# Performance work log

Measured on AMD Instinct MI355X. Metric: run time of the kernel, lower is better.

## Reference

```python
import jax, jax.numpy as jnp
import numpy as np

B, S, D, H, HD, C = 4, 1024, 1024, 16, 64, 64
NC = S // C
DFF = 4 * HD
BASE_LR = 1.0
EPS = 1e-6

def _ln(x, g, b, eps=EPS):
    mu = jnp.mean(x, axis=-1, keepdims=True)
    var = jnp.mean((x - mu) ** 2, axis=-1, keepdims=True)
    return (x - mu) * jax.lax.rsqrt(var + eps) * g + b

def _gelu(x):
    return 0.5 * x * (1.0 + jnp.tanh(0.79788456 * (x + 0.044715 * x * x * x)))

def _gelu_bwd(x):
    t = jnp.tanh(0.79788456 * (x + 0.044715 * x * x * x))
    return 0.5 * x * (1.0 - t * t) * (0.79788456 + 0.1070322243 * x * x) + 0.5 * (1.0 + t)

def _ln_l2_bwd(x, tgt, g, b, eps=EPS):
    # grad of 0.5*||LN_affine(x) - tgt||^2 w.r.t. x (fused layernorm backward)
    d = x.shape[-1]
    mu = jnp.mean(x, axis=-1, keepdims=True)
    var = jnp.mean((x - mu) ** 2, axis=-1, keepdims=True)
    std = jnp.sqrt(var + eps)
    xh = (x - mu) / std
    gh = (g * xh + b - tgt) * g
    return (d * gh - jnp.sum(gh, axis=-1, keepdims=True) - xh * jnp.sum(gh * xh, axis=-1, keepdims=True)) / (d * std)

def setup_inputs():
    key = jax.random.key(0)
    ks = jax.random.split(key, 16)
    n = lambda k, shape, s=0.02: jax.random.normal(k, shape, dtype=jnp.float32) * s
    return {
        "x": jax.random.normal(ks[0], (B, S, D), dtype=jnp.float32),
        "ln1_w": jnp.ones((D,), jnp.float32), "ln1_b": jnp.zeros((D,), jnp.float32),
        "attn_wq": n(ks[1], (D, D)), "attn_wk": n(ks[2], (D, D)),
        "attn_wv": n(ks[3], (D, D)), "attn_wo": n(ks[4], (D, D)),
        "wq_w": n(ks[5], (D, D)), "wq_b": jnp.zeros((D,), jnp.float32),
        "wk_w": n(ks[6], (D, D)), "wk_b": jnp.zeros((D,), jnp.float32),
        "wv_w": n(ks[7], (D, D)), "wv_b": jnp.zeros((D,), jnp.float32),
        "wo_w": n(ks[8], (D, D)), "wo_b": jnp.zeros((D,), jnp.float32),
        "W1": n(ks[9], (H, HD, DFF)), "b1": jnp.zeros((H, 1, DFF), jnp.float32),
        "W2": n(ks[10], (H, DFF, HD)), "b2": jnp.zeros((H, 1, HD), jnp.float32),
        "ttt_nw": jnp.ones((H, HD), jnp.float32), "ttt_nb": jnp.zeros((H, HD), jnp.float32),
        "lr_w": n(ks[11], (H, 1, D)), "lr_b": jnp.zeros((H, 1), jnp.float32),
        "pn_w": jnp.ones((D,), jnp.float32), "pn_b": jnp.zeros((D,), jnp.float32),
        "gate_alpha": n(ks[12], (D,)),
    }

def reference(x, ln1_w, ln1_b, attn_wq, attn_wk, attn_wv, attn_wo,
              wq_w, wq_b, wk_w, wk_b, wv_w, wv_b, wo_w, wo_b,
              W1, b1, W2, b2, ttt_nw, ttt_nb, lr_w, lr_b, pn_w, pn_b, gate_alpha):
    # ---- self-attention block (pre-norm, causal, residual) ----
    h = _ln(x, ln1_w, ln1_b)
    q = (h @ attn_wq.T).reshape(B, S, H, HD)
    k = (h @ attn_wk.T).reshape(B, S, H, HD)
    v = (h @ attn_wv.T).reshape(B, S, H, HD)
    scores = jnp.einsum('bqhd,bkhd->bhqk', q, k) / jnp.float32(np.sqrt(HD))
    causal = jnp.tril(jnp.ones((S, S), bool))
    scores = jnp.where(causal, scores, jnp.float32(-1e30))
    o = jnp.einsum('bhqk,bkhd->bqhd', jax.nn.softmax(scores, axis=-1), v).reshape(B, S, D)
    x = x + o @ attn_wo.T

    # ---- TTT-MLP chunked inner-loop (Video-DiT style) ----
    residual = x
    XQ = (x @ wq_w.T + wq_b).reshape(B, S, H, HD)
    XK = (x @ wk_w.T + wk_b).reshape(B, S, H, HD)
    XV = (x @ wv_w.T + wv_b).reshape(B, S, H, HD)
    XQ = XQ / jnp.maximum(jnp.linalg.norm(XQ, axis=-1, keepdims=True), 1e-12)
    XK = XK / jnp.maximum(jnp.linalg.norm(XK, axis=-1, keepdims=True), 1e-12)
    # ln reconstruction target: affine-LN(XV) + XK
    XV = ttt_nw[None, None] * _ln(XV, 1.0, 0.0) + ttt_nb[None, None] + XK

    to_ttt = lambda t: jnp.moveaxis(t.reshape(B, NC, C, H, HD), 3, 1)  # [B,H,NC,C,HD]
    XQc, XKc, XVc = to_ttt(XQ), to_ttt(XK), to_ttt(XV)

    xc = x.reshape(B, NC, C, D)
    ttt_lr = jax.nn.sigmoid(jnp.einsum('bnkc,hdc->bhnkd', xc, lr_w) + lr_b.reshape(1, H, 1, 1, 1))
    eta = BASE_LR * jnp.swapaxes(ttt_lr, -1, -2) / HD  # [B,H,NC,1,C]

    gW = ttt_nw[None, :, None, :]
    gB = ttt_nb[None, :, None, :]

    def step(carry, inp):
        W1s, b1s, W2s, b2s = carry
        xq, xk, xv, et = inp                          # [B,H,C,HD], et [B,H,1,C]
        eta_mb = jnp.broadcast_to(et, (B, H, C, C))
        Z1 = xk @ W1s + b1s                           # [B,H,C,DFF]
        X2 = _gelu(Z1)
        Z2 = X2 @ W2s + b2s                           # [B,H,C,HD]
        gZ2 = _ln_l2_bwd(Z2, xv - xk, gW, gB)
        gZ1 = (gZ2 @ jnp.swapaxes(W2s, -1, -2)) * _gelu_bwd(Z1)
        eta_tril = jnp.tril(eta_mb)
        A1 = jnp.tril(xq @ jnp.swapaxes(xk, -1, -2))
        Z1b = xq @ W1s - (eta_mb * A1) @ gZ1 + (b1s - eta_tril @ gZ1)
        X2b = _gelu(Z1b)
        A2 = jnp.tril(X2b @ jnp.swapaxes(X2, -1, -2))
        Z2b = X2b @ W2s - (eta_mb * A2) @ gZ2 + (b2s - eta_tril @ gZ2)
        last = eta_mb[:, :, -1, :, None]              # [B,H,C,1]
        W1n = W1s - jnp.swapaxes(last * xk, -1, -2) @ gZ1
        b1n = b1s - jnp.sum(last * gZ1, axis=-2, keepdims=True)
        W2n = W2s - jnp.swapaxes(last * X2, -1, -2) @ gZ2
        b2n = b2s - jnp.sum(last * gZ2, axis=-2, keepdims=True)
        out = xq + _ln(Z2b, gW, gB)
        return (W1n, b1n, W2n, b2n), out

    carry = (jnp.broadcast_to(W1, (B, H, HD, DFF)), jnp.broadcast_to(b1, (B, H, 1, DFF)),
             jnp.broadcast_to(W2, (B, H, DFF, HD)), jnp.broadcast_to(b2, (B, H, 1, HD)))
    xs = tuple(jnp.moveaxis(t, 2, 0) for t in (XQc, XKc, XVc, eta))
    _, outs = jax.lax.scan(step, carry, xs)           # [NC,B,H,C,HD]
    ttt_out = outs.transpose(1, 0, 3, 2, 4).reshape(B, S, D)

    z = _ln(ttt_out, pn_w, pn_b) @ wo_w.T + wo_b      # post-norm then output proj
    return residual + jnp.tanh(gate_alpha) * z        # SSM gating + gated residual
```

## Files before the change

kernel.cpp:

```cpp
#include <hip/hip_runtime.h>

typedef short v8s __attribute__((ext_vector_type(8)));
typedef short v4s __attribute__((ext_vector_type(4)));
typedef float v4f __attribute__((ext_vector_type(4)));

__device__ __forceinline__ float bfu(unsigned short u){ return __uint_as_float(((unsigned)u)<<16); }
__device__ __forceinline__ unsigned short fbf(float f){
  unsigned u = __float_as_uint(f);
  u += 0x7fffu + ((u>>16)&1u);
  return (unsigned short)(u>>16);
}
__device__ __forceinline__ float wsum(float v){
  #pragma unroll
  for (int off=32; off>0; off>>=1) v += __shfl_xor(v, off, 64);
  return v;
}
__device__ __forceinline__ float clampv(float x){ return fminf(fmaxf(x, -1e8f), 1e8f); }
__device__ __forceinline__ float tanh_f(float x){
  x = fminf(fmaxf(x, -15.f), 15.f);
  float e = __expf(2.f*x);
  return (e-1.f)/(e+1.f);
}
__device__ __forceinline__ float gelu_f(float x){
  float t = tanh_f(0.79788456f*(x + 0.044715f*x*x*x));
  return 0.5f*x*(1.f+t);
}
__device__ __forceinline__ float gelu_bwd_f(float x){
  float t = tanh_f(0.79788456f*(x + 0.044715f*x*x*x));
  return 0.5f*x*(1.f-t*t)*(0.79788456f + 0.1070322243f*x*x) + 0.5f*(1.f+t);
}
__device__ __forceinline__ v8s ld8(const unsigned short* p){
  v4s lo = *(const v4s*)p, hi = *(const v4s*)(p+4);
  v8s r;
  r[0]=lo[0];r[1]=lo[1];r[2]=lo[2];r[3]=lo[3];
  r[4]=hi[0];r[5]=hi[1];r[6]=hi[2];r[7]=hi[3];
  return r;
}

__global__ __launch_bounds__(256) void wcvt_kernel(
    const float* __restrict__ s0, const float* __restrict__ s1, const float* __restrict__ s2,
    unsigned short* __restrict__ d0, unsigned short* __restrict__ d1, unsigned short* __restrict__ d2)
{
  int y = blockIdx.y;
  const float* s = y==0?s0:(y==1?s1:s2);
  unsigned short* d = y==0?d0:(y==1?d1:d2);
  int tid = blockIdx.x*256 + threadIdx.x;
  #pragma unroll 4
  for (int i=0;i<16;i++){
    size_t o = (size_t)i*65536 + (size_t)tid*4;
    float4 v = *(const float4*)&s[o];
    v4s p;
    p[0]=(short)fbf(v.x); p[1]=(short)fbf(v.y); p[2]=(short)fbf(v.z); p[3]=(short)fbf(v.w);
    *(v4s*)&d[o] = p;
  }
}

__global__ __launch_bounds__(256) void ln_kernel(
    const float* __restrict__ X, const float* __restrict__ g,
    const float* __restrict__ bta, float* __restrict__ out,
    unsigned short* __restrict__ outbf)
{
  __shared__ float red[4];
  int row = blockIdx.x, t = threadIdx.x;
  const float* xr = X + (size_t)row*1024;
  float v[4];
  #pragma unroll
  for (int i=0;i<4;i++) v[i] = xr[t + i*256];
  float s = v[0]+v[1]+v[2]+v[3];
  s = wsum(s);
  if ((t&63)==0) red[t>>6]=s;
  __syncthreads();
  float mu = (red[0]+red[1]+red[2]+red[3])*(1.f/1024.f);
  float q=0.f;
  #pragma unroll
  for (int i=0;i<4;i++){ float dd=v[i]-mu; q+=dd*dd; }
  q = wsum(q);
  __syncthreads();
  if ((t&63)==0) red[t>>6]=q;
  __syncthreads();
  float var = (red[0]+red[1]+red[2]+red[3])*(1.f/1024.f);
  float rs = rsqrtf(var+1e-6f);
  #pragma unroll
  for (int i=0;i<4;i++){
    int c = t+i*256;
    float vv = (v[i]-mu)*rs*g[c] + bta[c];
    if (out)   out[(size_t)row*1024+c] = vv;
    if (outbf) outbf[(size_t)row*1024+c] = fbf(vv);
  }
}

__global__ __launch_bounds__(256, 2) void gemm_kernel(
    const unsigned short* __restrict__ A_bf,
    const unsigned short* __restrict__ B0, const unsigned short* __restrict__ B1, const unsigned short* __restrict__ B2,
    const float* __restrict__ bias0, const float* __restrict__ bias1, const float* __restrict__ bias2,
    const float* __restrict__ res, const float* __restrict__ gate,
    float* __restrict__ out0, float* __restrict__ out1, float* __restrict__ out2,
    unsigned short* __restrict__ obf0, unsigned short* __restrict__ obf1, unsigned short* __restrict__ obf2)
{
  __shared__ __attribute__((aligned(16))) unsigned short a_lds[128*68];
  __shared__ __attribute__((aligned(16))) unsigned short b_lds[128*68];
  int t=threadIdx.x, w=t>>6, lane=t&63;
  int widx = blockIdx.x>>3;
  const unsigned short* Bw = widx==0?B0:(widx==1?B1:B2);
  const float* bias = widx==0?bias0:(widx==1?bias1:bias2);
  float* out        = widx==0?out0:(widx==1?out1:out2);
  unsigned short* obf = widx==0?obf0:(widx==1?obf1:obf2);
  int gm = blockIdx.y*128, gn = (blockIdx.x&7)*128;
  int wm=(w>>1)*64, wn=(w&1)*64, lr=lane&15, lk=(lane>>4)*8;
  v4f acc[4][4];
  #pragma unroll
  for (int i=0;i<4;i++)
    #pragma unroll
    for (int j=0;j<4;j++){ v4f z={0.f,0.f,0.f,0.f}; acc[i][j]=z; }
  for (int kk=0; kk<1024; kk+=64){
    __syncthreads();
    #pragma unroll
    for (int i=0;i<4;i++){
      int slot=i*256+t, row=slot>>3, c8=(slot&7)*8;
      const unsigned short* srcA=&A_bf[(size_t)(gm+row)*1024 + kk + c8];
      v4s lo=*(const v4s*)srcA, hi=*(const v4s*)(srcA+4);
      *(v4s*)&a_lds[row*68+c8]   = lo;
      *(v4s*)&a_lds[row*68+c8+4] = hi;
      const unsigned short* srcB=&Bw[(size_t)(gn+row)*1024 + kk + c8];
      v4s blo=*(const v4s*)srcB, bhi=*(const v4s*)(srcB+4);
      *(v4s*)&b_lds[row*68+c8]   = blo;
      *(v4s*)&b_lds[row*68+c8+4] = bhi;
    }
    __syncthreads();
    #pragma unroll
    for (int k2=0;k2<2;k2++){
      v8s af[4], bfr[4];
      #pragma unroll
      for (int i=0;i<4;i++) af[i] = ld8(&a_lds[(wm+i*16+lr)*68 + k2*32+lk]);
      #pragma unroll
      for (int j=0;j<4;j++) bfr[j] = ld8(&b_lds[(wn+j*16+lr)*68 + k2*32+lk]);
      #pragma unroll
      for (int i=0;i<4;i++)
        #pragma unroll
        for (int j=0;j<4;j++)
          acc[i][j] = __builtin_amdgcn_mfma_f32_16x16x32_bf16(af[i], bfr[j], acc[i][j], 0,0,0);
    }
  }
  int quad = lane>>4;
  #pragma unroll
  for (int j=0;j<4;j++){
    int gc = gn + wn + j*16 + lr;
    float bval = bias ? bias[gc] : 0.f;
    float gval = gate ? tanh_f(gate[gc]) : 1.f;
    #pragma unroll
    for (int i=0;i<4;i++){
      #pragma unroll
      for (int r=0;r<4;r++){
        int grow = gm + wm + i*16 + quad*4 + r;
        float v = (acc[i][j][r] + bval)*gval;
        if (res) v += res[(size_t)grow*1024 + gc];
        size_t oi = (size_t)grow*1024 + gc;
        if (out) out[oi] = v;
        if (obf) obf[oi] = fbf(v);
      }
    }
  }
}

__global__ __launch_bounds__(256) void attn_kernel(
    const unsigned short* __restrict__ Q, const unsigned short* __restrict__ K,
    const unsigned short* __restrict__ V, float* __restrict__ O,
    unsigned short* __restrict__ Obf)
{
  __shared__ __attribute__((aligned(16))) unsigned short q_l[64*68];
  __shared__ __attribute__((aligned(16))) unsigned short k_l[64*68];
  __shared__ __attribute__((aligned(16))) unsigned short vt_l[64*68];
  __shared__ __attribute__((aligned(16))) unsigned short p_l[64*68];
  int t=threadIdx.x, w=t>>6, lane=t&63, q=lane>>4, l16=lane&15;
  int qt = blockIdx.x & 15, bh = blockIdx.x >> 4;
  int b = bh >> 4, h = bh & 15;
  const size_t base = ((size_t)b*1024)*1024 + (size_t)h*64;
  #pragma unroll
  for (int pass=0;pass<4;pass++){
    int slot=t+pass*256, row=slot>>4, c4=(slot&15)*4;
    v4s qv = *(const v4s*)&Q[base + (size_t)(qt*64+row)*1024 + c4];
    *(v4s*)&q_l[row*68+c4]=qv;
  }
  float mi[4], li[4];
  v4f o[4];
  #pragma unroll
  for (int r=0;r<4;r++){ mi[r]=-1e30f; li[r]=0.f; }
  #pragma unroll
  for (int dtn=0;dtn<4;dtn++){ v4f z={0.f,0.f,0.f,0.f}; o[dtn]=z; }
  for (int kt=0; kt<=qt; kt++){
    __syncthreads();
    #pragma unroll
    for (int pass=0;pass<4;pass++){
      int slot=t+pass*256, row=slot>>4, c4=(slot&15)*4;
      v4s kv = *(const v4s*)&K[base + (size_t)(kt*64+row)*1024 + c4];
      *(v4s*)&k_l[row*68+c4]=kv;
      v4s vv = *(const v4s*)&V[base + (size_t)(kt*64+row)*1024 + c4];
      vt_l[(c4+0)*68+row]=(unsigned short)vv[0];
      vt_l[(c4+1)*68+row]=(unsigned short)vv[1];
      vt_l[(c4+2)*68+row]=(unsigned short)vv[2];
      vt_l[(c4+3)*68+row]=(unsigned short)vv[3];
    }
    __syncthreads();
    v4f s[4];
    #pragma unroll
    for (int nt=0;nt<4;nt++){ v4f z={0.f,0.f,0.f,0.f}; s[nt]=z; }
    #pragma unroll
    for (int k2=0;k2<2;k2++){
      v8s af = ld8(&q_l[(w*16+l16)*68 + k2*32+q*8]);
      #pragma unroll
      for (int nt=0;nt<4;nt++){
        v8s bf = ld8(&k_l[(nt*16+l16)*68 + k2*32+q*8]);
        s[nt] = __builtin_amdgcn_mfma_f32_16x16x32_bf16(af, bf, s[nt], 0,0,0);
      }
    }
    bool diag = (kt==qt);
    #pragma unroll
    for (int r=0;r<4;r++){
      int row_l = w*16+q*4+r;
      float mx=-1e30f;
      #pragma unroll
      for (int nt=0;nt<4;nt++){
        int col=nt*16+l16;
        float sv = s[nt][r]*0.125f;
        if (diag && col>row_l) sv=-1e30f;
        s[nt][r]=sv; mx=fmaxf(mx,sv);
      }
      #pragma unroll
      for (int off=1;off<16;off<<=1) mx=fmaxf(mx,__shfl_xor(mx,off,16));
      float mnew=fmaxf(mi[r],mx);
      float aexp=__expf(mi[r]-mnew);
      float ps=0.f;
      #pragma unroll
      for (int nt=0;nt<4;nt++){
        float p=__expf(s[nt][r]-mnew);
        s[nt][r]=p; ps+=p;
      }
      #pragma unroll
      for (int off=1;off<16;off<<=1) ps+=__shfl_xor(ps,off,16);
      li[r]=li[r]*aexp+ps; mi[r]=mnew;
      #pragma unroll
      for (int dtn=0;dtn<4;dtn++) o[dtn][r]*=aexp;
      #pragma unroll
      for (int nt=0;nt<4;nt++) p_l[row_l*68 + nt*16+l16]=fbf(s[nt][r]);
    }
    __syncthreads();
    #pragma unroll
    for (int k2=0;k2<2;k2++){
      v8s af = ld8(&p_l[(w*16+l16)*68 + k2*32+q*8]);
      #pragma unroll
      for (int dtn=0;dtn<4;dtn++){
        v8s bf = ld8(&vt_l[(dtn*16+l16)*68 + k2*32+q*8]);
        o[dtn] = __builtin_amdgcn_mfma_f32_16x16x32_bf16(af, bf, o[dtn], 0,0,0);
      }
    }
  }
  #pragma unroll
  for (int dtn=0;dtn<4;dtn++)
    #pragma unroll
    for (int r=0;r<4;r++){
      float vv = o[dtn][r]/li[r];
      size_t oi = base + (size_t)(qt*64+w*16+q*4+r)*1024 + dtn*16+l16;
      if (O)   O[oi] = vv;
      if (Obf) Obf[oi] = fbf(vv);
    }
}

__global__ __launch_bounds__(256) void xqkv_kernel(
    const float* __restrict__ XQ, const float* __restrict__ XK,
    const float* __restrict__ XV, const float* __restrict__ nw,
    const float* __restrict__ nb, const float* __restrict__ eta,
    float* __restrict__ xqt, float* __restrict__ tgtp,
    unsigned short* __restrict__ xq_bf, unsigned short* __restrict__ xk_bf,
    unsigned short* __restrict__ xkTe_bf)
{
  int gw = (int)((blockIdx.x*256 + threadIdx.x)>>6);
  int lane = threadIdx.x & 63;
  int h = gw & 15, s = (gw>>4)&1023, b = gw>>14;
  size_t src = ((size_t)(b*1024+s))*1024 + h*64 + lane;
  float xq = XQ[src], xk = XK[src], xv = XV[src];
  float nq = sqrtf(wsum(xq*xq));
  float nk = sqrtf(wsum(xk*xk));
  float xqn = xq / fmaxf(nq, 1e-12f);
  float xkn = xk / fmaxf(nk, 1e-12f);
  float mu = wsum(xv)*(1.f/64.f);
  float xm = xv-mu;
  float var = wsum(xm*xm)*(1.f/64.f);
  float xvh = xm*rsqrtf(var+1e-6f);
  float tg = nw[h*64+lane]*xvh + nb[h*64+lane];
  float et = eta[((size_t)(b*16+h))*1024 + s];
  size_t dst = ((size_t)(b*16+h)*1024 + s)*64 + lane;
  xq_bf[dst]=fbf(xqn); xk_bf[dst]=fbf(xkn);
  xkTe_bf[((size_t)(b*16+h)*64 + lane)*1024 + s] = fbf(-et*xkn);
  int n_ = s>>6, row = s&63;
  int wv = row>>4, qq = (row>>2)&3, rr = row&3;
  int nt_ = lane>>4, l16_ = lane&15;
  int tt = wv*64 + qq*16 + l16_;
  size_t dst2 = (size_t)(b*16+h)*65536 + (size_t)n_*4096 + (size_t)tt*16 + nt_*4 + rr;
  xqt[dst2]=xqn; tgtp[dst2]=tg;
}

__global__ __launch_bounds__(256) void eta_kernel(
    const float* __restrict__ Xb, const float* __restrict__ lrw,
    const float* __restrict__ lrb, float* __restrict__ eta)
{
  int gw = (int)((blockIdx.x*256 + threadIdx.x)>>6);
  int lane = threadIdx.x & 63;
  int s = gw & 1023, b = gw >> 10;
  const float* xrow = Xb + ((size_t)(b*1024+s))*1024;
  float xr[16];
  #pragma unroll
  for (int i=0;i<16;i++) xr[i] = xrow[i*64+lane];
  #pragma unroll 1
  for (int h=0;h<16;h++){
    const float* wr = lrw + h*1024;
    float acc=0.f;
    #pragma unroll
    for (int i=0;i<16;i++) acc += xr[i]*wr[i*64+lane];
    acc = wsum(acc);
    if (lane==h){
      float vv = acc + lrb[h];
      float sg = 1.f/(1.f+__expf(-vv));
      eta[((size_t)(b*16+h))*1024 + s] = sg*(1.f/64.f);
    }
  }
}

__global__ __launch_bounds__(512, 2) __attribute__((amdgpu_waves_per_eu(2, 2)))
void scan_kernel(
    const float* __restrict__ xqt, const float* __restrict__ tgtp,
    const unsigned short* __restrict__ xq_bf, const unsigned short* __restrict__ xk_bf,
    const unsigned short* __restrict__ xkTe_bf, const float* __restrict__ eta,
    const float* __restrict__ W1in, const float* __restrict__ b1in,
    const float* __restrict__ W2in, const float* __restrict__ b2in,
    const float* __restrict__ nw, const float* __restrict__ nb,
    float* __restrict__ tout)
{
  __shared__ __attribute__((aligned(16))) unsigned short W1t[256*68];
  __shared__ __attribute__((aligned(16))) unsigned short W2T[64*260];
  __shared__ __attribute__((aligned(16))) unsigned short X2s[64*260];
  __shared__ __attribute__((aligned(16))) unsigned short GXu[256*68];
  __shared__ __attribute__((aligned(16))) unsigned short GZ2t[64*68];
  __shared__ __attribute__((aligned(16))) unsigned short AMs[64*68];
  __shared__ float ln_scr[64*8];
  __shared__ float eta_s[64], b1_s[256], b2_s[64], nw_s[64], nb_s[64];

  const int t=threadIdx.x, w=t>>6, lane=t&63, q=lane>>4, l16=lane&15;
  const int bh=blockIdx.x, b=bh>>4, h=bh&15;
  const int mt=w>>1, half=w&1, nh=half*8, nh4=half*2;
  const float* xq_g  = xqt  + (size_t)bh*65536;
  const float* tgt_g = tgtp + (size_t)bh*65536;
  const unsigned short* xqb_g = xq_bf  + (size_t)bh*65536;
  const unsigned short* xkb_g = xk_bf  + (size_t)bh*65536;
  const unsigned short* xkT_g = xkTe_bf + (size_t)bh*65536;
  const float* eta_g = eta + (size_t)bh*1024;

  v4f w1r[8];
  #pragma unroll
  for (int nt=0;nt<8;nt++){
    int col=(nh+nt)*16+l16;
    #pragma unroll
    for (int r=0;r<4;r++) w1r[nt][r] = W1in[h*16384 + (mt*16+q*4+r)*256 + col];
  }
  v4f w2r[2][4];
  #pragma unroll
  for (int mi=0;mi<2;mi++)
    #pragma unroll
    for (int nt=0;nt<4;nt++){
      int col=nt*16+l16;
      #pragma unroll
      for (int r=0;r<4;r++) w2r[mi][nt][r] = W2in[h*16384 + ((w*2+mi)*16+q*4+r)*64 + col];
    }
  if (t<256) b1_s[t]=b1in[h*256+t];
  if (t<64){ b2_s[t]=b2in[h*64+t]; nw_s[t]=nw[h*64+t]; nb_s[t]=nb[h*64+t]; }

  float bacc=0.f, bacc2=0.f;

  for (int n=0;n<16;n++){
    v8s xkf[2], xqf[2];
    #pragma unroll
    for (int kt=0;kt<2;kt++){
      xkf[kt] = ld8(&xkb_g[(size_t)n*4096 + (mt*16+l16)*64 + kt*32+q*8]);
      xqf[kt] = ld8(&xqb_g[(size_t)n*4096 + (mt*16+l16)*64 + kt*32+q*8]);
    }
    __syncthreads();
    if (t<256) b1_s[t] -= bacc;
    if (t<64){ b2_s[t] -= bacc2; eta_s[t]=eta_g[n*64+t]; }
    #pragma unroll
    for (int nt=0;nt<8;nt++){
      int col=(nh+nt)*16+l16;
      #pragma unroll
      for (int pr=0;pr<2;pr++){
        unsigned lo=fbf(w1r[nt][pr*2]), hi=fbf(w1r[nt][pr*2+1]);
        *(unsigned*)&W1t[col*68 + mt*16+q*4 + pr*2] = lo | (hi<<16);
      }
    }
    #pragma unroll
    for (int mi=0;mi<2;mi++)
      #pragma unroll
      for (int nt=0;nt<4;nt++){
        int col=nt*16+l16;
        #pragma unroll
        for (int pr=0;pr<2;pr++){
          unsigned lo=fbf(w2r[mi][nt][pr*2]), hi=fbf(w2r[mi][nt][pr*2+1]);
          *(unsigned*)&W2T[col*260 + (w*2+mi)*16+q*4 + pr*2] = lo | (hi<<16);
        }
      }
    __syncthreads();

    unsigned gbp[16];
    {
      v4f a1[8];
      #pragma unroll
      for (int i=0;i<8;i++){ v4f z={0.f,0.f,0.f,0.f}; a1[i]=z; }
      #pragma unroll
      for (int kt=0;kt<2;kt++){
        #pragma unroll
        for (int nt=0;nt<8;nt++){
          v8s bf = ld8(&W1t[((nh+nt)*16+l16)*68 + kt*32+q*8]);
          a1[nt] = __builtin_amdgcn_mfma_f32_16x16x32_bf16(xkf[kt], bf, a1[nt], 0,0,0);
        }
      }
      #pragma unroll
      for (int nt=0;nt<8;nt++){
        int col=(nh+nt)*16+l16; float bb=b1_s[col];
        float zz[4];
        #pragma unroll
        for (int r=0;r<4;r++){
          float z=clampv(a1[nt][r]+bb); zz[r]=z;
          X2s[(mt*16+q*4+r)*260+col]=fbf(clampv(gelu_f(z)));
        }
        #pragma unroll
        for (int pr=0;pr<2;pr++)
          gbp[nt*2+pr] = (unsigned)fbf(gelu_bwd_f(zz[pr*2+0]))
                       | ((unsigned)fbf(gelu_bwd_f(zz[pr*2+1]))<<16);
      }
    }
    {
      v4f a4[2];
      #pragma unroll
      for (int i=0;i<2;i++){ v4f z={0.f,0.f,0.f,0.f}; a4[i]=z; }
      #pragma unroll
      for (int kt=0;kt<2;kt++){
        #pragma unroll
        for (int nt=0;nt<2;nt++){
          v8s bf = ld8(&xkb_g[(size_t)n*4096 + ((nh4+nt)*16+l16)*64 + kt*32+q*8]);
          a4[nt] = __builtin_amdgcn_mfma_f32_16x16x32_bf16(xqf[kt], bf, a4[nt], 0,0,0);
        }
      }
      #pragma unroll
      for (int nt=0;nt<2;nt++){
        int col=(nh4+nt)*16+l16;
        float ec=eta_s[col];
        #pragma unroll
        for (int r=0;r<4;r++){
          int row=mt*16+q*4+r;
          AMs[row*68+col] = (col<=row) ? fbf(-ec*(a4[nt][r]+1.f)) : (unsigned short)0;
        }
      }
    }

    {
      const float* tc = tgt_g + (size_t)n*4096 + (size_t)(mt*64+q*16+l16)*16 + nh4*4;
      float4 ta=*(const float4*)tc, tb=*(const float4*)(tc+4);
      float tgs[8]={ta.x,ta.y,ta.z,ta.w,tb.x,tb.y,tb.z,tb.w};
      v4f a2[2];
      #pragma unroll
      for (int i=0;i<2;i++){ v4f z={0.f,0.f,0.f,0.f}; a2[i]=z; }
      #pragma unroll
      for (int kt=0;kt<8;kt++){
        v8s af = ld8(&X2s[(mt*16+l16)*260 + kt*32+q*8]);
        #pragma unroll
        for (int nt=0;nt<2;nt++){
          v8s bf = ld8(&W2T[((nh4+nt)*16+l16)*260 + kt*32+q*8]);
          a2[nt] = __builtin_amdgcn_mfma_f32_16x16x32_bf16(af, bf, a2[nt], 0,0,0);
        }
      }
      float z2[2][4];
      #pragma unroll
      for (int nt=0;nt<2;nt++){
        float bb=b2_s[(nh4+nt)*16+l16];
        #pragma unroll
        for (int r=0;r<4;r++) z2[nt][r]=clampv(a2[nt][r]+bb);
      }
      #pragma unroll
      for (int r=0;r<4;r++){
        float s1v=z2[0][r]+z2[1][r];
        float s2v=z2[0][r]*z2[0][r]+z2[1][r]*z2[1][r];
        #pragma unroll
        for (int off=1;off<16;off<<=1){ s1v+=__shfl_xor(s1v,off,16); s2v+=__shfl_xor(s2v,off,16); }
        if (l16==0){ int row=mt*16+q*4+r; ln_scr[row*8+half]=s1v; ln_scr[row*8+2+half]=s2v; }
      }
      __syncthreads();
      float muv[4], istd[4];
      #pragma unroll
      for (int r=0;r<4;r++){
        int row=mt*16+q*4+r;
        float S1=ln_scr[row*8+0]+ln_scr[row*8+1];
        float S2=ln_scr[row*8+2]+ln_scr[row*8+3];
        float mu=S1*(1.f/64.f);
        float var=fmaxf(S2*(1.f/64.f)-mu*mu, 0.f);
        muv[r]=mu; istd[r]=rsqrtf(var+1e-6f);
      }
      float xh[2][4], gh[2][4];
      #pragma unroll
      for (int nt=0;nt<2;nt++){
        int col=(nh4+nt)*16+l16;
        float gw_=nw_s[col], gb_=nb_s[col];
        #pragma unroll
        for (int r=0;r<4;r++){
          float x_=(z2[nt][r]-muv[r])*istd[r];
          float tgv = tgs[nt*4+r];
          xh[nt][r]=x_;
          gh[nt][r]=(gw_*x_+gb_-tgv)*gw_;
        }
      }
      #pragma unroll
      for (int r=0;r<4;r++){
        float t1=gh[0][r]+gh[1][r];
        float t2=gh[0][r]*xh[0][r]+gh[1][r]*xh[1][r];
        #pragma unroll
        for (int off=1;off<16;off<<=1){ t1+=__shfl_xor(t1,off,16); t2+=__shfl_xor(t2,off,16); }
        if (l16==0){ int row=mt*16+q*4+r; ln_scr[row*8+4+half]=t1; ln_scr[row*8+6+half]=t2; }
      }
      __syncthreads();
      #pragma unroll
      for (int nt=0;nt<2;nt++){
        int col=(nh4+nt)*16+l16;
        #pragma unroll
        for (int pr=0;pr<2;pr++){
          unsigned pk[2];
          #pragma unroll
          for (int k2=0;k2<2;k2++){
            int r=pr*2+k2;
            int row=mt*16+q*4+r;
            float G1s=ln_scr[row*8+4]+ln_scr[row*8+5];
            float G2s=ln_scr[row*8+6]+ln_scr[row*8+7];
            float gz=(64.f*gh[nt][r]-G1s-xh[nt][r]*G2s)*istd[r]*(1.f/64.f);
            pk[k2]=fbf(clampv(gz));
          }
          *(unsigned*)&GZ2t[col*68 + mt*16+q*4 + pr*2] = pk[0] | (pk[1]<<16);
        }
      }
    }
    __syncthreads();

    {
      v4f a3[8];
      #pragma unroll
      for (int i=0;i<8;i++){ v4f z={0.f,0.f,0.f,0.f}; a3[i]=z; }
      #pragma unroll
      for (int kt=0;kt<2;kt++){
        v8s af;
        #pragma unroll
        for (int j=0;j<8;j++) af[j]=(short)GZ2t[(kt*32+q*8+j)*68 + mt*16+l16];
        #pragma unroll
        for (int nt=0;nt<8;nt++){
          int nb0=(nh+nt)*16+l16;
          v8s bf;
          #pragma unroll
          for (int j=0;j<8;j++) bf[j]=(short)W2T[(kt*32+q*8+j)*260 + nb0];
          a3[nt] = __builtin_amdgcn_mfma_f32_16x16x32_bf16(af, bf, a3[nt], 0,0,0);
        }
      }
      #pragma unroll
      for (int nt=0;nt<8;nt++){
        int col=(nh+nt)*16+l16;
        #pragma unroll
        for (int pr=0;pr<2;pr++){
          float d0=bfu((unsigned short)(gbp[nt*2+pr]&0xffffu));
          float d1=bfu((unsigned short)(gbp[nt*2+pr]>>16));
          float g0=clampv(a3[nt][pr*2+0]*d0);
          float g1=clampv(a3[nt][pr*2+1]*d1);
          unsigned lo=fbf(g0), hi=fbf(g1);
          *(unsigned*)&GXu[col*68 + mt*16+q*4 + pr*2] = lo | (hi<<16);
        }
      }
    }
    __syncthreads();

    unsigned x2bp[16];
    {
      float p0=0.f,p1=0.f,p2=0.f,p3=0.f;
      if (t<256){
        #pragma unroll
        for (int j4=0;j4<16;j4++){
          v4s v=*(const v4s*)&GXu[t*68+j4*4];
          p0 += eta_s[j4*4+0]*bfu((unsigned short)v[0]);
          p1 += eta_s[j4*4+1]*bfu((unsigned short)v[1]);
          p2 += eta_s[j4*4+2]*bfu((unsigned short)v[2]);
          p3 += eta_s[j4*4+3]*bfu((unsigned short)v[3]);
        }
      }
      bacc=(p0+p1)+(p2+p3);
      v8s xef[2];
      #pragma unroll
      for (int kt=0;kt<2;kt++)
        xef[kt] = ld8(&xkT_g[(size_t)(mt*16+l16)*1024 + n*64 + kt*32+q*8]);
      v4f a5[8];
      #pragma unroll
      for (int i=0;i<8;i++){ v4f z={0.f,0.f,0.f,0.f}; a5[i]=z; }
      #pragma unroll
      for (int kt=0;kt<2;kt++){
        #pragma unroll
        for (int nt=0;nt<8;nt++){
          v8s bf = ld8(&W1t[((nh+nt)*16+l16)*68 + kt*32+q*8]);
          a5[nt] = __builtin_amdgcn_mfma_f32_16x16x32_bf16(xqf[kt], bf, a5[nt], 0,0,0);
        }
      }
      #pragma unroll
      for (int kt=0;kt<2;kt++){
        v8s afA = ld8(&AMs[(mt*16+l16)*68 + kt*32+q*8]);
        #pragma unroll
        for (int nt=0;nt<8;nt++){
          v8s bf = ld8(&GXu[((nh+nt)*16+l16)*68 + kt*32+q*8]);
          a5[nt] = __builtin_amdgcn_mfma_f32_16x16x32_bf16(afA, bf, a5[nt], 0,0,0);
          w1r[nt] = __builtin_amdgcn_mfma_f32_16x16x32_bf16(xef[kt], bf, w1r[nt], 0,0,0);
        }
      }
      #pragma unroll
      for (int nt=0;nt<8;nt++){
        float bb=b1_s[(nh+nt)*16+l16];
        #pragma unroll
        for (int pr=0;pr<2;pr++){
          float z0=clampv(a5[nt][pr*2+0]+bb);
          float z1=clampv(a5[nt][pr*2+1]+bb);
          x2bp[nt*2+pr] = (unsigned)fbf(clampv(gelu_f(z0)))
                        | ((unsigned)fbf(clampv(gelu_f(z1)))<<16);
        }
      }
    }
    __syncthreads();

    #pragma unroll
    for (int nt=0;nt<8;nt++){
      int col=(nh+nt)*16+l16;
      #pragma unroll
      for (int pr=0;pr<2;pr++){
        int row0=mt*16+q*4+pr*2;
        GXu[row0*260+col]     = (unsigned short)(x2bp[nt*2+pr]&0xffffu);
        GXu[(row0+1)*260+col] = (unsigned short)(x2bp[nt*2+pr]>>16);
      }
    }
    __syncthreads();

    {
      float p0=0.f,p1=0.f,p2=0.f,p3=0.f;
      if (t<64){
        #pragma unroll
        for (int j4=0;j4<16;j4++){
          v4s v=*(const v4s*)&GZ2t[t*68+j4*4];
          p0 += eta_s[j4*4+0]*bfu((unsigned short)v[0]);
          p1 += eta_s[j4*4+1]*bfu((unsigned short)v[1]);
          p2 += eta_s[j4*4+2]*bfu((unsigned short)v[2]);
          p3 += eta_s[j4*4+3]*bfu((unsigned short)v[3]);
        }
      }
      bacc2=(p0+p1)+(p2+p3);
      v4f a7[2];
      #pragma unroll
      for (int i=0;i<2;i++){ v4f z={0.f,0.f,0.f,0.f}; a7[i]=z; }
      #pragma unroll
      for (int kt=0;kt<8;kt++){
        v8s af = ld8(&GXu[(mt*16+l16)*260 + kt*32+q*8]);
        #pragma unroll
        for (int nt=0;nt<2;nt++){
          v8s bf = ld8(&X2s[((nh4+nt)*16+l16)*260 + kt*32+q*8]);
          a7[nt] = __builtin_amdgcn_mfma_f32_16x16x32_bf16(af, bf, a7[nt], 0,0,0);
        }
      }
      #pragma unroll
      for (int nt=0;nt<2;nt++){
        int col=(nh4+nt)*16+l16;
        float ec=eta_s[col];
        #pragma unroll
        for (int r=0;r<4;r++){
          int row=mt*16+q*4+r;
          AMs[row*68+col] = (col<=row) ? fbf(-ec*(a7[nt][r]+1.f)) : (unsigned short)0;
        }
      }
    }
    __syncthreads();

    {
      const float* xc = xq_g + (size_t)n*4096 + (size_t)(mt*64+q*16+l16)*16 + nh4*4;
      float4 xa=*(const float4*)xc, xb=*(const float4*)(xc+4);
      float xqs[8]={xa.x,xa.y,xa.z,xa.w,xb.x,xb.y,xb.z,xb.w};
      v4f a8[2];
      #pragma unroll
      for (int i=0;i<2;i++){ v4f z={0.f,0.f,0.f,0.f}; a8[i]=z; }
      float b2old[2];
      #pragma unroll
      for (int nt=0;nt<2;nt++) b2old[nt]=b2_s[(nh4+nt)*16+l16];
      #pragma unroll
      for (int kt=0;kt<8;kt++){
        v8s af = ld8(&GXu[(mt*16+l16)*260 + kt*32+q*8]);
        #pragma unroll
        for (int nt=0;nt<2;nt++){
          v8s bf = ld8(&W2T[((nh4+nt)*16+l16)*260 + kt*32+q*8]);
          a8[nt] = __builtin_amdgcn_mfma_f32_16x16x32_bf16(af, bf, a8[nt], 0,0,0);
        }
      }
      #pragma unroll
      for (int kt=0;kt<2;kt++){
        v8s afm = ld8(&AMs[(mt*16+l16)*68 + kt*32+q*8]);
        #pragma unroll
        for (int nt=0;nt<2;nt++){
          v8s bf = ld8(&GZ2t[((nh4+nt)*16+l16)*68 + kt*32+q*8]);
          a8[nt] = __builtin_amdgcn_mfma_f32_16x16x32_bf16(afm, bf, a8[nt], 0,0,0);
        }
      }
      float z2b[2][4];
      #pragma unroll
      for (int nt=0;nt<2;nt++)
        #pragma unroll
        for (int r=0;r<4;r++) z2b[nt][r]=clampv(a8[nt][r]+b2old[nt]);
      #pragma unroll
      for (int r=0;r<4;r++){
        float s1v=z2b[0][r]+z2b[1][r];
        float s2v=z2b[0][r]*z2b[0][r]+z2b[1][r]*z2b[1][r];
        #pragma unroll
        for (int off=1;off<16;off<<=1){ s1v+=__shfl_xor(s1v,off,16); s2v+=__shfl_xor(s2v,off,16); }
        if (l16==0){ int row=mt*16+q*4+r; ln_scr[row*8+half]=s1v; ln_scr[row*8+2+half]=s2v; }
      }
      __syncthreads();
      #pragma unroll
      for (int r=0;r<4;r++){
        int row=mt*16+q*4+r;
        float S1=ln_scr[row*8+0]+ln_scr[row*8+1];
        float S2=ln_scr[row*8+2]+ln_scr[row*8+3];
        float mu=S1*(1.f/64.f);
        float var=fmaxf(S2*(1.f/64.f)-mu*mu, 0.f);
        float istd=rsqrtf(var+1e-6f);
        #pragma unroll
        for (int nt=0;nt<2;nt++){
          int col=(nh4+nt)*16+l16;
          float x_=(z2b[nt][r]-mu)*istd;
          float outv = xqs[nt*4+r] + x_*nw_s[col] + nb_s[col];
          tout[((size_t)(b*1024 + n*64 + row))*1024 + h*64 + col] = outv;
        }
      }
      #pragma unroll
      for (int kt=0;kt<2;kt++){
        v8s bfs[4];
        #pragma unroll
        for (int nt=0;nt<4;nt++) bfs[nt] = ld8(&GZ2t[(nt*16+l16)*68 + kt*32+q*8]);
        #pragma unroll
        for (int mi=0;mi<2;mi++){
          v8s af;
          #pragma unroll
          for (int j=0;j<8;j++){
            int jj=kt*32+q*8+j;
            af[j]=(short)fbf(-eta_s[jj]*bfu(X2s[jj*260 + (w*2+mi)*16+l16]));
          }
          #pragma unroll
          for (int nt=0;nt<4;nt++)
            w2r[mi][nt] = __builtin_amdgcn_mfma_f32_16x16x32_bf16(af, bfs[nt], w2r[mi][nt], 0,0,0);
        }
      }
    }
  }
}

extern "C" void kernel_launch(void* const* d_in, const int* in_sizes, int n_in,
                              void* d_out, int out_size, void* d_ws, size_t ws_size,
                              hipStream_t stream)
{
  const float* x_in   = (const float*)d_in[0];
  const float* ln1w   = (const float*)d_in[1];
  const float* ln1b   = (const float*)d_in[2];
  const float* awq    = (const float*)d_in[3];
  const float* awk    = (const float*)d_in[4];
  const float* awv    = (const float*)d_in[5];
  const float* awo    = (const float*)d_in[6];
  const float* wqw    = (const float*)d_in[7];
  const float* wqb    = (const float*)d_in[8];
  const float* wkw    = (const float*)d_in[9];
  const float* wkb    = (const float*)d_in[10];
  const float* wvw    = (const float*)d_in[11];
  const float* wvb    = (const float*)d_in[12];
  const float* wow    = (const float*)d_in[13];
  const float* wob    = (const float*)d_in[14];
  const float* W1in   = (const float*)d_in[15];
  const float* b1in   = (const float*)d_in[16];
  const float* W2in   = (const float*)d_in[17];
  const float* b2in   = (const float*)d_in[18];
  const float* tnw    = (const float*)d_in[19];
  const float* tnb    = (const float*)d_in[20];
  const float* lrw    = (const float*)d_in[21];
  const float* lrb    = (const float*)d_in[22];
  const float* pnw    = (const float*)d_in[23];
  const float* pnb    = (const float*)d_in[24];
  const float* galpha = (const float*)d_in[25];
  float* outp = (float*)d_out;
  char* ws = (char*)d_ws;
  const size_t MB = (size_t)1<<20;
  float* bq  = (float*)(ws + 0*MB);
  float* bk  = (float*)(ws + 16*MB);
  float* bv  = (float*)(ws + 32*MB);
  float* bo  = (float*)(ws + 64*MB);
  float* bxb = (float*)(ws + 80*MB);
  float* xqt = (float*)(ws + 96*MB);
  float* tgtp = (float*)(ws + 112*MB);
  unsigned short* xq_bf  = (unsigned short*)(ws + 128*MB);
  unsigned short* xk_bf  = (unsigned short*)(ws + 136*MB);
  float* etab = (float*)(ws + 144*MB);
  unsigned short* xkTe_bf = (unsigned short*)(ws + 48*MB);
  unsigned short* wc0 = (unsigned short*)(ws + 56*MB);
  unsigned short* wc1 = (unsigned short*)(ws + 58*MB);
  unsigned short* wc2 = (unsigned short*)(ws + 60*MB);
  unsigned short* bhh_bf  = (unsigned short*)(ws + 96*MB);
  unsigned short* bq_bf   = (unsigned short*)(ws + 128*MB);
  unsigned short* bk_bf   = (unsigned short*)(ws + 136*MB);
  unsigned short* bv_bf   = (unsigned short*)(ws + 80*MB);
  unsigned short* bo_bf   = (unsigned short*)(ws + 112*MB);
  unsigned short* bxb_bf  = (unsigned short*)(ws + 128*MB);
  unsigned short* bhh2_bf = (unsigned short*)(ws + 0*MB);
  float* tout = bo;

  wcvt_kernel<<<dim3(64,3),256,0,stream>>>(awq,awk,awv, wc0,wc1,wc2);
  ln_kernel<<<4096,256,0,stream>>>(x_in, ln1w, ln1b, nullptr, bhh_bf);
  gemm_kernel<<<dim3(24,32),256,0,stream>>>(bhh_bf, wc0,wc1,wc2,
      nullptr,nullptr,nullptr, nullptr, nullptr,
      nullptr,nullptr,nullptr, bq_bf,bk_bf,bv_bf);
  wcvt_kernel<<<dim3(64,1),256,0,stream>>>(awo,nullptr,nullptr, wc0,nullptr,nullptr);
  attn_kernel<<<1024,256,0,stream>>>(bq_bf,bk_bf,bv_bf, nullptr, bo_bf);
  gemm_kernel<<<dim3(8,32),256,0,stream>>>(bo_bf, wc0,wc0,wc0,
      nullptr,nullptr,nullptr, x_in, nullptr,
      bxb,bxb,bxb, bxb_bf,bxb_bf,bxb_bf);
  wcvt_kernel<<<dim3(64,3),256,0,stream>>>(wqw,wkw,wvw, wc0,wc1,wc2);
  gemm_kernel<<<dim3(24,32),256,0,stream>>>(bxb_bf, wc0,wc1,wc2,
      wqb,wkb,wvb, nullptr, nullptr,
      bq,bk,bv, nullptr,nullptr,nullptr);
  wcvt_kernel<<<dim3(64,1),256,0,stream>>>(wow,nullptr,nullptr, wc0,nullptr,nullptr);
  eta_kernel<<<1024,256,0,stream>>>(bxb, lrw, lrb, etab);
  xqkv_kernel<<<16384,256,0,stream>>>(bq,bk,bv,tnw,tnb,etab,xqt,tgtp,xq_bf,xk_bf,xkTe_bf);
  scan_kernel<<<64,512,0,stream>>>(xqt,tgtp,xq_bf,xk_bf,xkTe_bf,etab,W1in,b1in,W2in,b2in,tnw,tnb,tout);
  ln_kernel<<<4096,256,0,stream>>>(tout, pnw, pnb, nullptr, bhh2_bf);
  gemm_kernel<<<dim3(8,32),256,0,stream>>>(bhh2_bf, wc0,wc0,wc0,
      wob,wob,wob, bxb, galpha,
      outp,outp,outp, nullptr,nullptr,nullptr);
}
```

Measured before the change: 926.7 us.

## Fuse scan layernorm-backward reductions into one pass and merge weight conversions

The layernorm-backward in the sequential scan kernel is rewritten algebraically so the row sums needed for the gradient (sum of gh and gh*xhat) come from raw moments gathered in the same shuffle reduction as mean and variance. This removes a second shuffle reduction and one block barrier per chunk. The change also hoists the target, xq and transposed-xk loads to the top of each chunk iteration, computes tanh once for both GELU and its derivative, and merges the separate output-weight conversion launches into the four-way convert kernels. The trade-off is slightly different floating-point rounding from the expanded moment formulas, plus higher register pressure from the hoisted loads.

```diff
diff --git a/kernel.cpp b/kernel.cpp
--- a/kernel.cpp
+++ b/kernel.cpp
@@ -38,12 +38,14 @@
 }
 
 __global__ __launch_bounds__(256) void wcvt_kernel(
-    const float* __restrict__ s0, const float* __restrict__ s1, const float* __restrict__ s2,
-    unsigned short* __restrict__ d0, unsigned short* __restrict__ d1, unsigned short* __restrict__ d2)
+    const float* __restrict__ s0, const float* __restrict__ s1,
+    const float* __restrict__ s2, const float* __restrict__ s3,
+    unsigned short* __restrict__ d0, unsigned short* __restrict__ d1,
+    unsigned short* __restrict__ d2, unsigned short* __restrict__ d3)
 {
   int y = blockIdx.y;
-  const float* s = y==0?s0:(y==1?s1:s2);
-  unsigned short* d = y==0?d0:(y==1?d1:d2);
+  const float* s = y==0?s0:(y==1?s1:(y==2?s2:s3));
+  unsigned short* d = y==0?d0:(y==1?d1:(y==2?d2:d3));
   int tid = blockIdx.x*256 + threadIdx.x;
   #pragma unroll 4
   for (int i=0;i<16;i++){
@@ -341,7 +343,7 @@
   __shared__ __attribute__((aligned(16))) unsigned short GXu[256*68];
   __shared__ __attribute__((aligned(16))) unsigned short GZ2t[64*68];
   __shared__ __attribute__((aligned(16))) unsigned short AMs[64*68];
-  __shared__ float ln_scr[64*8];
+  __shared__ float ln_scr[64*12];
   __shared__ float eta_s[64], b1_s[256], b2_s[64], nw_s[64], nb_s[64];
 
   const int t=threadIdx.x, w=t>>6, lane=t&63, q=lane>>4, l16=lane&15;
@@ -372,15 +374,31 @@
     }
   if (t<256) b1_s[t]=b1in[h*256+t];
   if (t<64){ b2_s[t]=b2in[h*64+t]; nw_s[t]=nw[h*64+t]; nb_s[t]=nb[h*64+t]; }
+  __syncthreads();
+  float T2g=0.f;
+  #pragma unroll
+  for (int c=0;c<64;c++){ float g=nw_s[c]; T2g += g*g; }
 
   float bacc=0.f, bacc2=0.f;
 
   for (int n=0;n<16;n++){
-    v8s xkf[2], xqf[2];
+    v8s xkf[2], xqf[2], xef[2];
     #pragma unroll
     for (int kt=0;kt<2;kt++){
       xkf[kt] = ld8(&xkb_g[(size_t)n*4096 + (mt*16+l16)*64 + kt*32+q*8]);
       xqf[kt] = ld8(&xqb_g[(size_t)n*4096 + (mt*16+l16)*64 + kt*32+q*8]);
+      xef[kt] = ld8(&xkT_g[(size_t)(mt*16+l16)*1024 + n*64 + kt*32+q*8]);
+    }
+    float tgs[8], xqs[8];
+    {
+      const float* tc = tgt_g + (size_t)n*4096 + (size_t)(mt*64+q*16+l16)*16 + nh4*4;
+      float4 ta=*(const float4*)tc, tb=*(const float4*)(tc+4);
+      tgs[0]=ta.x;tgs[1]=ta.y;tgs[2]=ta.z;tgs[3]=ta.w;
+      tgs[4]=tb.x;tgs[5]=tb.y;tgs[6]=tb.z;tgs[7]=tb.w;
+      const float* xc = xq_g + (size_t)n*4096 + (size_t)(mt*64+q*16+l16)*16 + nh4*4;
+      float4 xa=*(const float4*)xc, xb=*(const float4*)(xc+4);
+      xqs[0]=xa.x;xqs[1]=xa.y;xqs[2]=xa.z;xqs[3]=xa.w;
+      xqs[4]=xb.x;xqs[5]=xb.y;xqs[6]=xb.z;xqs[7]=xb.w;
     }
     __syncthreads();
     if (t<256) b1_s[t] -= bacc;
@@ -423,16 +441,18 @@
       #pragma unroll
       for (int nt=0;nt<8;nt++){
         int col=(nh+nt)*16+l16; float bb=b1_s[col];
-        float zz[4];
+        unsigned short dbf[4];
         #pragma unroll
         for (int r=0;r<4;r++){
-          float z=clampv(a1[nt][r]+bb); zz[r]=z;
-          X2s[(mt*16+q*4+r)*260+col]=fbf(clampv(gelu_f(z)));
-        }
-        #pragma unroll
-        for (int pr=0;pr<2;pr++)
-          gbp[nt*2+pr] = (unsigned)fbf(gelu_bwd_f(zz[pr*2+0]))
-                       | ((unsigned)fbf(gelu_bwd_f(zz[pr*2+1]))<<16);
+          float z=clampv(a1[nt][r]+bb);
+          float tt = tanh_f(0.79788456f*(z + 0.044715f*z*z*z));
+          float ge = 0.5f*z*(1.f+tt);
+          float gd = 0.5f*z*(1.f-tt*tt)*(0.79788456f + 0.1070322243f*z*z) + 0.5f*(1.f+tt);
+          X2s[(mt*16+q*4+r)*260+col]=fbf(clampv(ge));
+          dbf[r]=fbf(gd);
+        }
+        gbp[nt*2+0] = (unsigned)dbf[0] | ((unsigned)dbf[1]<<16);
+        gbp[nt*2+1] = (unsigned)dbf[2] | ((unsigned)dbf[3]<<16);
       }
     }
     {
@@ -460,9 +480,6 @@
     }
 
     {
-      const float* tc = tgt_g + (size_t)n*4096 + (size_t)(mt*64+q*16+l16)*16 + nh4*4;
-      float4 ta=*(const float4*)tc, tb=*(const float4*)(tc+4);
-      float tgs[8]={ta.x,ta.y,ta.z,ta.w,tb.x,tb.y,tb.z,tb.w};
       v4f a2[2];
       #pragma unroll
       for (int i=0;i<2;i++){ v4f z={0.f,0.f,0.f,0.f}; a2[i]=z; }
@@ -476,70 +493,57 @@
         }
       }
       float z2[2][4];
-      #pragma unroll
-      for (int nt=0;nt<2;nt++){
-        float bb=b2_s[(nh4+nt)*16+l16];
-        #pragma unroll
-        for (int r=0;r<4;r++) z2[nt][r]=clampv(a2[nt][r]+bb);
+      float gw0=nw_s[(nh4+0)*16+l16], gw1=nw_s[(nh4+1)*16+l16];
+      float gb0=nb_s[(nh4+0)*16+l16], gb1=nb_s[(nh4+1)*16+l16];
+      float gw20=gw0*gw0, gw21=gw1*gw1;
+      {
+        float bb0=b2_s[(nh4+0)*16+l16], bb1=b2_s[(nh4+1)*16+l16];
+        #pragma unroll
+        for (int r=0;r<4;r++){ z2[0][r]=clampv(a2[0][r]+bb0); z2[1][r]=clampv(a2[1][r]+bb1); }
       }
       #pragma unroll
       for (int r=0;r<4;r++){
-        float s1v=z2[0][r]+z2[1][r];
-        float s2v=z2[0][r]*z2[0][r]+z2[1][r]*z2[1][r];
-        #pragma unroll
-        for (int off=1;off<16;off<<=1){ s1v+=__shfl_xor(s1v,off,16); s2v+=__shfl_xor(s2v,off,16); }
-        if (l16==0){ int row=mt*16+q*4+r; ln_scr[row*8+half]=s1v; ln_scr[row*8+2+half]=s2v; }
+        float z0=z2[0][r], z1=z2[1][r];
+        float a0=gw0*(gb0-tgs[r]), a1v=gw1*(gb1-tgs[4+r]);
+        float s1=z0+z1, s2=z0*z0+z1*z1;
+        float t1=gw20*z0+gw21*z1;
+        float t4=gw20*z0*z0+gw21*z1*z1;
+        float t3=a0+a1v;
+        float t5=a0*z0+a1v*z1;
+        #pragma unroll
+        for (int off=1;off<16;off<<=1){
+          s1+=__shfl_xor(s1,off,16); s2+=__shfl_xor(s2,off,16);
+          t1+=__shfl_xor(t1,off,16); t4+=__shfl_xor(t4,off,16);
+          t3+=__shfl_xor(t3,off,16); t5+=__shfl_xor(t5,off,16);
+        }
+        if (l16==0){
+          int row=mt*16+q*4+r;
+          float* p=&ln_scr[row*12+half*6];
+          p[0]=s1; p[1]=s2; p[2]=t1; p[3]=t4; p[4]=t3; p[5]=t5;
+        }
       }
       __syncthreads();
-      float muv[4], istd[4];
       #pragma unroll
       for (int r=0;r<4;r++){
         int row=mt*16+q*4+r;
-        float S1=ln_scr[row*8+0]+ln_scr[row*8+1];
-        float S2=ln_scr[row*8+2]+ln_scr[row*8+3];
+        const float* p=&ln_scr[row*12];
+        float S1=p[0]+p[6], S2=p[1]+p[7], T1=p[2]+p[8], T4=p[3]+p[9], T3=p[4]+p[10], T5=p[5]+p[11];
         float mu=S1*(1.f/64.f);
         float var=fmaxf(S2*(1.f/64.f)-mu*mu, 0.f);
-        muv[r]=mu; istd[r]=rsqrtf(var+1e-6f);
-      }
-      float xh[2][4], gh[2][4];
-      #pragma unroll
-      for (int nt=0;nt<2;nt++){
-        int col=(nh4+nt)*16+l16;
-        float gw_=nw_s[col], gb_=nb_s[col];
-        #pragma unroll
-        for (int r=0;r<4;r++){
-          float x_=(z2[nt][r]-muv[r])*istd[r];
-          float tgv = tgs[nt*4+r];
-          xh[nt][r]=x_;
-          gh[nt][r]=(gw_*x_+gb_-tgv)*gw_;
-        }
-      }
-      #pragma unroll
-      for (int r=0;r<4;r++){
-        float t1=gh[0][r]+gh[1][r];
-        float t2=gh[0][r]*xh[0][r]+gh[1][r]*xh[1][r];
-        #pragma unroll
-        for (int off=1;off<16;off<<=1){ t1+=__shfl_xor(t1,off,16); t2+=__shfl_xor(t2,off,16); }
-        if (l16==0){ int row=mt*16+q*4+r; ln_scr[row*8+4+half]=t1; ln_scr[row*8+6+half]=t2; }
-      }
-      __syncthreads();
-      #pragma unroll
-      for (int nt=0;nt<2;nt++){
-        int col=(nh4+nt)*16+l16;
-        #pragma unroll
-        for (int pr=0;pr<2;pr++){
-          unsigned pk[2];
-          #pragma unroll
-          for (int k2=0;k2<2;k2++){
-            int r=pr*2+k2;
-            int row=mt*16+q*4+r;
-            float G1s=ln_scr[row*8+4]+ln_scr[row*8+5];
-            float G2s=ln_scr[row*8+6]+ln_scr[row*8+7];
-            float gz=(64.f*gh[nt][r]-G1s-xh[nt][r]*G2s)*istd[r]*(1.f/64.f);
-            pk[k2]=fbf(clampv(gz));
-          }
-          *(unsigned*)&GZ2t[col*68 + mt*16+q*4 + pr*2] = pk[0] | (pk[1]<<16);
-        }
+        float istd=rsqrtf(var+1e-6f);
+        float G1=istd*(T1-mu*T2g)+T3;
+        float G2=istd*istd*(T4-2.f*mu*T1+mu*mu*T2g)+istd*(T5-mu*T3);
+        unsigned short pk[2];
+        #pragma unroll
+        for (int nt=0;nt<2;nt++){
+          float gw_= nt? gw1:gw0, gb_= nt? gb1:gb0;
+          float x_=(z2[nt][r]-mu)*istd;
+          float gh=(gw_*x_+gb_-tgs[nt*4+r])*gw_;
+          float gz=(64.f*gh-G1-x_*G2)*istd*(1.f/64.f);
+          pk[nt]=fbf(clampv(gz));
+        }
+        GZ2t[((nh4+0)*16+l16)*68 + row] = pk[0];
+        GZ2t[((nh4+1)*16+l16)*68 + row] = pk[1];
       }
     }
     __syncthreads();
@@ -592,10 +596,6 @@
         }
       }
       bacc=(p0+p1)+(p2+p3);
-      v8s xef[2];
-      #pragma unroll
-      for (int kt=0;kt<2;kt++)
-        xef[kt] = ld8(&xkT_g[(size_t)(mt*16+l16)*1024 + n*64 + kt*32+q*8]);
       v4f a5[8];
       #pragma unroll
       for (int i=0;i<8;i++){ v4f z={0.f,0.f,0.f,0.f}; a5[i]=z; }
@@ -682,9 +682,6 @@
     __syncthreads();
 
     {
-      const float* xc = xq_g + (size_t)n*4096 + (size_t)(mt*64+q*16+l16)*16 + nh4*4;
-      float4 xa=*(const float4*)xc, xb=*(const float4*)(xc+4);
-      float xqs[8]={xa.x,xa.y,xa.z,xa.w,xb.x,xb.y,xb.z,xb.w};
       v4f a8[2];
       #pragma unroll
       for (int i=0;i<2;i++){ v4f z={0.f,0.f,0.f,0.f}; a8[i]=z; }
@@ -720,14 +717,14 @@
         float s2v=z2b[0][r]*z2b[0][r]+z2b[1][r]*z2b[1][r];
         #pragma unroll
         for (int off=1;off<16;off<<=1){ s1v+=__shfl_xor(s1v,off,16); s2v+=__shfl_xor(s2v,off,16); }
-        if (l16==0){ int row=mt*16+q*4+r; ln_scr[row*8+half]=s1v; ln_scr[row*8+2+half]=s2v; }
+        if (l16==0){ int row=mt*16+q*4+r; ln_scr[row*12+half]=s1v; ln_scr[row*12+2+half]=s2v; }
       }
       __syncthreads();
       #pragma unroll
       for (int r=0;r<4;r++){
         int row=mt*16+q*4+r;
-        float S1=ln_scr[row*8+0]+ln_scr[row*8+1];
-        float S2=ln_scr[row*8+2]+ln_scr[row*8+3];
+        float S1=ln_scr[row*12+0]+ln_scr[row*12+1];
+        float S2=ln_scr[row*12+2]+ln_scr[row*12+3];
         float mu=S1*(1.f/64.f);
         float var=fmaxf(S2*(1.f/64.f)-mu*mu, 0.f);
         float istd=rsqrtf(var+1e-6f);
@@ -808,6 +805,7 @@
   unsigned short* wc0 = (unsigned short*)(ws + 56*MB);
   unsigned short* wc1 = (unsigned short*)(ws + 58*MB);
   unsigned short* wc2 = (unsigned short*)(ws + 60*MB);
+  unsigned short* wc3 = (unsigned short*)(ws + 62*MB);
   unsigned short* bhh_bf  = (unsigned short*)(ws + 96*MB);
   unsigned short* bq_bf   = (unsigned short*)(ws + 128*MB);
   unsigned short* bk_bf   = (unsigned short*)(ws + 136*MB);
@@ -817,26 +815,24 @@
   unsigned short* bhh2_bf = (unsigned short*)(ws + 0*MB);
   float* tout = bo;
 
-  wcvt_kernel<<<dim3(64,3),256,0,stream>>>(awq,awk,awv, wc0,wc1,wc2);
+  wcvt_kernel<<<dim3(64,4),256,0,stream>>>(awq,awk,awv,awo, wc0,wc1,wc2,wc3);
   ln_kernel<<<4096,256,0,stream>>>(x_in, ln1w, ln1b, nullptr, bhh_bf);
   gemm_kernel<<<dim3(24,32),256,0,stream>>>(bhh_bf, wc0,wc1,wc2,
       nullptr,nullptr,nullptr, nullptr, nullptr,
       nullptr,nullptr,nullptr, bq_bf,bk_bf,bv_bf);
-  wcvt_kernel<<<dim3(64,1),256,0,stream>>>(awo,nullptr,nullptr, wc0,nullptr,nullptr);
   attn_kernel<<<1024,256,0,stream>>>(bq_bf,bk_bf,bv_bf, nullptr, bo_bf);
-  gemm_kernel<<<dim3(8,32),256,0,stream>>>(bo_bf, wc0,wc0,wc0,
+  gemm_kernel<<<dim3(8,32),256,0,stream>>>(bo_bf, wc3,wc3,wc3,
       nullptr,nullptr,nullptr, x_in, nullptr,
       bxb,bxb,bxb, bxb_bf,bxb_bf,bxb_bf);
-  wcvt_kernel<<<dim3(64,3),256,0,stream>>>(wqw,wkw,wvw, wc0,wc1,wc2);
+  wcvt_kernel<<<dim3(64,4),256,0,stream>>>(wqw,wkw,wvw,wow, wc0,wc1,wc2,wc3);
   gemm_kernel<<<dim3(24,32),256,0,stream>>>(bxb_bf, wc0,wc1,wc2,
       wqb,wkb,wvb, nullptr, nullptr,
       bq,bk,bv, nullptr,nullptr,nullptr);
-  wcvt_kernel<<<dim3(64,1),256,0,stream>>>(wow,nullptr,nullptr, wc0,nullptr,nullptr);
   eta_kernel<<<1024,256,0,stream>>>(bxb, lrw, lrb, etab);
   xqkv_kernel<<<16384,256,0,stream>>>(bq,bk,bv,tnw,tnb,etab,xqt,tgtp,xq_bf,xk_bf,xkTe_bf);
   scan_kernel<<<64,512,0,stream>>>(xqt,tgtp,xq_bf,xk_bf,xkTe_bf,etab,W1in,b1in,W2in,b2in,tnw,tnb,tout);
   ln_kernel<<<4096,256,0,stream>>>(tout, pnw, pnb, nullptr, bhh2_bf);
-  gemm_kernel<<<dim3(8,32),256,0,stream>>>(bhh2_bf, wc0,wc0,wc0,
+  gemm_kernel<<<dim3(8,32),256,0,stream>>>(bhh2_bf, wc3,wc3,wc3,
       wob,wob,wob, bxb, galpha,
       outp,outp,outp, nullptr,nullptr,nullptr);
 }
```

Result: no change. 934.1 us (+0.8%).
